# Performance work log

Measured on AMD Instinct MI355X. Metric: run time of the kernel, lower is better.

Reference implementation:

```python
import jax, jax.numpy as jnp
from jax import lax
import numpy as np


def conv2d(x, w, pad):
    # x: NCHW, w: OIHW
    return lax.conv_general_dilated(x, w, (1, 1), [(pad, pad), (pad, pad)],
                                    dimension_numbers=("NCHW", "OIHW", "NCHW"))


def make_dct_dict(num_atoms, num_dims):
    i = np.arange(num_atoms)[:, None].astype(np.float64)
    n = np.arange(num_dims)[None, :].astype(np.float64)
    w = np.cos((2.0 * n + 1.0) * i * (np.pi / (2.0 * num_dims)))
    w = w / np.linalg.norm(w, axis=1, keepdims=True)
    return jnp.asarray(w.T, dtype=jnp.float32)  # [num_dims, num_atoms]


def setup_inputs() -> dict:
    key = jax.random.key(0)
    B, C, H, W = 8, 64, 64, 64      # C = num_dims
    A = 256                          # num_atoms
    ks = jax.random.split(key, 10)
    s = 0.05
    Dict = make_dct_dict(A, C)       # [C, A]
    L = jnp.sum(Dict ** 2)           # ||Dict||_F^2 (scalar parameter)
    return {
        "x": jax.random.normal(ks[0], (B, C, H, W), jnp.float32),
        "conv_w": jax.random.normal(ks[1], (A, C, 3, 3), jnp.float32) * s,
        "conv_b": jax.random.normal(ks[2], (A,), jnp.float32) * s,
        "res1_w1": jax.random.normal(ks[3], (A // 2, A, 3, 3), jnp.float32) * s,
        "res1_w2": jax.random.normal(ks[4], (A, A // 2, 1, 1), jnp.float32) * s,
        "res2_w1": jax.random.normal(ks[5], (A // 2, A, 3, 3), jnp.float32) * s,
        "res2_w2": jax.random.normal(ks[6], (A, A // 2, 1, 1), jnp.float32) * s,
        "ca_w1": jax.random.normal(ks[7], (A // 16, A), jnp.float32) * s,  # Linear(A, A//16)
        "ca_w2": jax.random.normal(ks[8], (A, A // 16), jnp.float32) * s,  # Linear(A//16, A)
        "sa_w": jax.random.normal(ks[9], (1, 2, 3, 3), jnp.float32) * s,
        "Dict": Dict,
        "L": L,
        "num_iters": 16,
    }


def reference(x, conv_w, conv_b, res1_w1, res1_w2, res2_w1, res2_w2,
              ca_w1, ca_w2, sa_w, Dict, L, num_iters):
    def res_block(h, w1, w2):
        t = conv2d(jax.nn.relu(h), w1, 1)
        t = conv2d(jax.nn.relu(t), w2, 0)
        return h + t

    l = conv2d(x, conv_w, 1) + conv_b[None, :, None, None]
    l = res_block(l, res1_w1, res1_w2)
    l = res_block(l, res2_w1, res2_w2)

    # CBAM: channel attention (shared MLP on avg/max pooled features)
    avg = jnp.mean(l, axis=(2, 3))  # [B, A]
    mx = jnp.max(l, axis=(2, 3))
    fc = lambda v: jax.nn.relu(v @ ca_w1.T) @ ca_w2.T
    l = l * jax.nn.sigmoid(fc(avg) + fc(mx))[:, :, None, None]
    # CBAM: spatial attention
    s2 = jnp.concatenate([jnp.mean(l, axis=1, keepdims=True),
                          jnp.max(l, axis=1, keepdims=True)], axis=1)  # [B,2,H,W]
    l = l * jax.nn.sigmoid(conv2d(s2, sa_w, 1))

    lam = jnp.transpose(l / L, (0, 2, 3, 1))   # [B,H,W,A] per-position thresholds
    xp = jnp.transpose(x, (0, 2, 3, 1))        # [B,H,W,C]

    A = Dict.shape[1]
    S = (jnp.eye(A, dtype=Dict.dtype) - (Dict.T @ Dict) / L).T  # [A,A]
    y = xp @ Dict                               # [B,H,W,A]
    yL = y / L

    soft = lambda v: jnp.sign(v) * jnp.maximum(jnp.abs(v) - lam, 0.0)

    z0 = soft(y)

    def step(z, _):
        return soft(z @ S + yL), None

    z, _ = lax.scan(step, z0, None, length=num_iters)
    x_recon = z @ Dict.T                        # [B,H,W,C]

    return (jnp.transpose(z, (0, 3, 1, 2)),
            jnp.transpose(x_recon, (0, 3, 1, 2)),
            Dict)
```

## Files before the change

### kernel.cpp

```cpp
#include <hip/hip_runtime.h>
#include <hip/hip_bf16.h>

typedef __attribute__((ext_vector_type(8))) short short8v;
typedef __attribute__((ext_vector_type(4))) short short4v;
typedef __attribute__((ext_vector_type(4))) float float4v;

__device__ __forceinline__ unsigned short f2bu(float v){
  __hip_bfloat16 h = __float2bfloat16(v);
  union { __hip_bfloat16 h; unsigned short u; } cv; cv.h = h; return cv.u;
}

__device__ __forceinline__ float softt(float v, float lam){
  float t = fmaxf(fabsf(v) - lam, 0.f);
  float r = copysignf(t, v);
  return (v == 0.f) ? 0.f : r;
}

__global__ void k_Lin(const float* __restrict__ Lsrc, float* __restrict__ Lb){
  Lb[0] = Lsrc[0];
}

__global__ void k_gram(const float* __restrict__ D, unsigned short* __restrict__ Gb){
  int j = blockIdx.x, a = threadIdx.x;
  float acc = 0.f;
  for (int c = 0; c < 64; ++c)
    acc += D[c*256 + j] * D[c*256 + a];
  Gb[j*256 + a] = f2bu(acc);
}

__global__ void k_transpD(const float* __restrict__ D, float* __restrict__ DT,
                          unsigned short* __restrict__ DTb){
  int gid = blockIdx.x * 256 + threadIdx.x;
  if (gid < 16384) {
    int a = gid >> 6, c = gid & 63;
    float v = D[c*256 + a];
    DT[gid] = v;
    DTb[gid] = f2bu(v);
  }
}

__global__ void k_castw(const float* __restrict__ w, unsigned short* __restrict__ wb,
                        int n){
  int gid = blockIdx.x * 256 + threadIdx.x;
  if (gid < n) wb[gid] = f2bu(w[gid]);
}

__global__ void k_permw3(const float* __restrict__ w, unsigned short* __restrict__ wb,
                         int logI, int n){
  int gid = blockIdx.x * 256 + threadIdx.x;
  if (gid >= n) return;
  int I = 1 << logI;
  int i = gid & (I - 1);
  int t = gid >> logI;
  int o = t / 9;
  int r = t - o * 9;
  wb[gid] = f2bu(w[((o << logI) + i) * 9 + r]);
}

template<int KS, int CIN, int BN, bool BIAS, bool RES, bool WF32, bool WBF>
__global__ __launch_bounds__(256) void k_conv(
    const unsigned short* __restrict__ in, const unsigned short* __restrict__ wb,
    const float* __restrict__ bias, const float* res, float* outf,
    unsigned short* __restrict__ outb, int Cout)
{
  constexpr int TPC   = CIN / 64;
  constexpr int K     = KS * KS * CIN;
  constexpr int LOGBN = (BN == 128) ? 7 : 6;
  constexpr int BCH   = BN / 32;
  constexpr int NT    = BN / 64;

  __shared__ unsigned short Asb[64][72];
  __shared__ unsigned short Bsb[BN][72];

  const int tid = threadIdx.x;
  int bx = blockIdx.x;
  { const int cpx = gridDim.x >> 3; bx = (bx & 7) * cpx + (bx >> 3); }
  const int m0  = bx * 64;
  const int n0  = blockIdx.y * BN;
  const int b   = m0 >> 12;
  const int hw0 = m0 & 4095;
  const int h   = hw0 >> 6;
  const int w0  = hw0 & 63;

  const int sm  = tid & 63;
  const int sq8 = tid >> 6;
  const int bn  = tid & (BN - 1);
  const int bq  = tid >> LOGBN;

  const int w   = tid >> 6;
  const int ln  = tid & 63;
  const int q   = ln >> 4;
  const int l16 = ln & 15;

  float4v acc[NT][4];
  #pragma unroll
  for (int nt = 0; nt < NT; ++nt)
    #pragma unroll
    for (int mt = 0; mt < 4; ++mt)
      acc[nt][mt] = (float4v){0.f, 0.f, 0.f, 0.f};

  int sA = 0, sB = TPC;
  if (KS == 3) { sA = (h == 0 ? 3 : 0) * TPC; sB = (h == 63 ? 6 : 9) * TPC; }

  short8v a_r0, a_r1;
  short8v b_r[4];

  auto pref = [&](int s){
    const int r   = s / TPC;
    const int c64 = s - r * TPC;
    int hh = h, ww = w0 + sm;
    bool ok = true;
    if (KS == 3) {
      const int r3 = r / 3;
      const int dw = r - r3 * 3 - 1;
      hh = h + r3 - 1;
      ww += dw;
      ok = ((unsigned)ww < 64u);
    }
    a_r0 = (short8v){0,0,0,0,0,0,0,0};
    a_r1 = (short8v){0,0,0,0,0,0,0,0};
    if (ok) {
      const unsigned short* ap = in +
          (((size_t)(b * CIN + c64 * 64 + sq8 * 8)) << 12) + (hh << 6) + ww;
      #pragma unroll
      for (int j = 0; j < 8; ++j)
        a_r0[j] = (short)ap[(size_t)j << 12];
      const unsigned short* ap2 = ap + ((size_t)32 << 12);
      #pragma unroll
      for (int j = 0; j < 8; ++j)
        a_r1[j] = (short)ap2[(size_t)j << 12];
    }
    const unsigned short* bp = wb + (size_t)(n0 + bn) * K + s * 64 + bq * (BCH * 8);
    #pragma unroll
    for (int j = 0; j < BCH; ++j)
      b_r[j] = *(const short8v*)(bp + j * 8);
  };

  pref(sA);
  for (int s = sA; s < sB; ) {
    *(short8v*)(&Asb[sm][sq8 * 8])       = a_r0;
    *(short8v*)(&Asb[sm][32 + sq8 * 8])  = a_r1;
    #pragma unroll
    for (int j = 0; j < BCH; ++j)
      *(short8v*)(&Bsb[bn][bq * (BCH * 8) + j * 8]) = b_r[j];
    __syncthreads();
    const int sn = s + 1;
    if (sn < sB) pref(sn);
    short8v Af[4][2];
    #pragma unroll
    for (int mt = 0; mt < 4; ++mt) {
      Af[mt][0] = *(const short8v*)(&Asb[mt * 16 + l16][q * 8]);
      Af[mt][1] = *(const short8v*)(&Asb[mt * 16 + l16][32 + q * 8]);
    }
    #pragma unroll
    for (int nt = 0; nt < NT; ++nt) {
      const int nr = w * (BN / 4) + nt * 16 + l16;
      const short8v Bf0 = *(const short8v*)(&Bsb[nr][q * 8]);
      const short8v Bf1 = *(const short8v*)(&Bsb[nr][32 + q * 8]);
      #pragma unroll
      for (int mt = 0; mt < 4; ++mt) {
        acc[nt][mt] = __builtin_amdgcn_mfma_f32_16x16x32_bf16(
            Af[mt][0], Bf0, acc[nt][mt], 0, 0, 0);
        acc[nt][mt] = __builtin_amdgcn_mfma_f32_16x16x32_bf16(
            Af[mt][1], Bf1, acc[nt][mt], 0, 0, 0);
      }
    }
    __syncthreads();
    s = sn;
  }

  #pragma unroll
  for (int nt = 0; nt < NT; ++nt) {
    const int n = n0 + w * (BN / 4) + nt * 16 + l16;
    float bv = 0.f;
    if (BIAS) bv = bias[n];
    #pragma unroll
    for (int mt = 0; mt < 4; ++mt) {
      const size_t base = (((size_t)(b * Cout + n)) << 12) + hw0 + mt * 16 + q * 4;
      float o[4];
      #pragma unroll
      for (int r2 = 0; r2 < 4; ++r2) o[r2] = acc[nt][mt][r2] + bv;
      if (RES) {
        float4 r4 = *(const float4*)(res + base);
        o[0] += r4.x; o[1] += r4.y; o[2] += r4.z; o[3] += r4.w;
      }
      if (WF32) {
        float4 o4; o4.x = o[0]; o4.y = o[1]; o4.z = o[2]; o4.w = o[3];
        *(float4*)(outf + base) = o4;
      }
      if (WBF) {
        short4v s4;
        #pragma unroll
        for (int r2 = 0; r2 < 4; ++r2) s4[r2] = (short)f2bu(fmaxf(o[r2], 0.f));
        *(short4v*)(outb + base) = s4;
      }
    }
  }
}

__global__ void k_pool(const float* __restrict__ l, float* __restrict__ avg,
                       float* __restrict__ mx){
  int b = blockIdx.y, a = blockIdx.x, tid = threadIdx.x;
  const float* p = l + ((size_t)(b * 256 + a) << 12);
  float s = 0.f, m = -1e30f;
  for (int i = tid; i < 4096; i += 256) { float v = p[i]; s += v; m = fmaxf(m, v); }
  __shared__ float ss[256], sm[256];
  ss[tid] = s; sm[tid] = m; __syncthreads();
  for (int o = 128; o > 0; o >>= 1) {
    if (tid < o) { ss[tid] += ss[tid+o]; sm[tid] = fmaxf(sm[tid], sm[tid+o]); }
    __syncthreads();
  }
  if (tid == 0) { avg[b*256+a] = ss[0] * (1.f/4096.f); mx[b*256+a] = sm[0]; }
}

__global__ void k_ca(const float* __restrict__ avg, const float* __restrict__ mx,
                     const float* __restrict__ w1, const float* __restrict__ w2,
                     float* __restrict__ cscale){
  int b = blockIdx.x, tid = threadIdx.x;
  __shared__ float h[16];
  if (tid < 16) {
    float sa = 0.f, sm = 0.f;
    for (int a = 0; a < 256; ++a) {
      float w = w1[tid*256 + a];
      sa += avg[b*256 + a] * w;
      sm += mx[b*256 + a] * w;
    }
    h[tid] = fmaxf(sa, 0.f) + fmaxf(sm, 0.f);
  }
  __syncthreads();
  float s = 0.f;
  for (int j = 0; j < 16; ++j) s += h[j] * w2[tid*16 + j];
  cscale[b*256 + tid] = 1.f / (1.f + __expf(-s));
}

__global__ void k_s2(const float* __restrict__ l, const float* __restrict__ cscale,
                     float* __restrict__ s2){
  int b = blockIdx.y;
  int hw = blockIdx.x * 256 + threadIdx.x;
  const float* p  = l + (((size_t)b * 256) << 12) + hw;
  const float* cs = cscale + b * 256;
  float s = 0.f, m = -1e30f;
  for (int a = 0; a < 256; ++a) {
    float v = p[(size_t)a << 12] * cs[a];
    s += v; m = fmaxf(m, v);
  }
  s2[((b*2) << 12) + hw]   = s * (1.f/256.f);
  s2[((b*2+1) << 12) + hw] = m;
}

__global__ void k_sa(const float* __restrict__ s2, const float* __restrict__ w,
                     float* __restrict__ sa){
  int b = blockIdx.y;
  int hw = blockIdx.x * 256 + threadIdx.x;
  int h = hw >> 6, ww = hw & 63;
  float acc = 0.f;
  for (int ch = 0; ch < 2; ++ch)
    for (int dh = -1; dh <= 1; ++dh)
      for (int dw = -1; dw <= 1; ++dw) {
        int hh = h + dh, wc = ww + dw;
        if ((unsigned)hh < 64u && (unsigned)wc < 64u)
          acc += s2[((b*2+ch) << 12) + (hh << 6) + wc] * w[ch*9 + (dh+1)*3 + (dw+1)];
      }
  sa[(b << 12) + hw] = 1.f / (1.f + __expf(-acc));
}

#define XTS 80

__device__ __forceinline__ int zoff(int pos, int au8){
  return pos * 256 + (((au8 ^ (pos & 15)) & 31) << 3);
}

__global__ __launch_bounds__(256, 2) void k_lista(
    const unsigned short* __restrict__ xb,
    const unsigned short* __restrict__ DTb,
    const unsigned short* __restrict__ Gb,
    const float* __restrict__ lmap, const float* __restrict__ csc,
    const float* __restrict__ sav, const float* __restrict__ Lb,
    float* __restrict__ zout)
{
  __shared__ unsigned short zbuf[2][16 * 256];

  const int tid = threadIdx.x;
  const int m0  = blockIdx.x * 16;
  const int b   = m0 >> 12;
  const int hw0 = m0 & 4095;
  const float invL = 1.0f / Lb[0];

  unsigned short* xTb = &zbuf[1][0];
  {
    const int i  = tid & 15;
    const int c0 = tid >> 4;
    #pragma unroll
    for (int cc = 0; cc < 4; ++cc) {
      int c = c0 + cc * 16;
      xTb[i * XTS + c] = xb[((b * 64 + c) << 12) + hw0 + i];
    }
  }

  const int w   = tid >> 6;
  const int ln  = tid & 63;
  const int q   = ln >> 4;
  const int l16 = ln & 15;

  short8v Sg[4][8];
  #pragma unroll
  for (int at = 0; at < 4; ++at)
    #pragma unroll
    for (int ks = 0; ks < 8; ++ks)
      Sg[at][ks] = *(const short8v*)(
          Gb + (size_t)(w * 64 + at * 16 + l16) * 256 + ks * 32 + q * 8);

  __syncthreads();

  float z[4][4], yl[4][4], lamr[4][4];

  {
    const short8v B0 = *(const short8v*)(&xTb[l16 * XTS + q * 8]);
    const short8v B1 = *(const short8v*)(&xTb[l16 * XTS + 32 + q * 8]);
    #pragma unroll
    for (int at = 0; at < 4; ++at) {
      const int abase = w * 64 + at * 16;
      const short8v A0 = *(const short8v*)(DTb + (abase + l16) * 64 + q * 8);
      const short8v A1 = *(const short8v*)(DTb + (abase + l16) * 64 + 32 + q * 8);
      float4v a = {0.f, 0.f, 0.f, 0.f};
      a = __builtin_amdgcn_mfma_f32_16x16x32_bf16(A0, B0, a, 0, 0, 0);
      a = __builtin_amdgcn_mfma_f32_16x16x32_bf16(A1, B1, a, 0, 0, 0);
      short4v pk;
      #pragma unroll
      for (int r = 0; r < 4; ++r) {
        const int atom = abase + q * 4 + r;
        const float lv = lmap[(((size_t)(b * 256 + atom)) << 12) + hw0 + l16];
        const float sv = sav[(b << 12) + hw0 + l16];
        const float cv = csc[b * 256 + atom];
        const float lm = ((lv * cv) * sv) * invL;
        const float yv = a[r];
        lamr[at][r] = lm;
        yl[at][r]   = yv * invL;
        const float z0 = softt(yv, lm);
        z[at][r] = z0;
        pk[r] = (short)f2bu(z0);
      }
      *(short4v*)(&zbuf[0][zoff(l16, w * 8 + at * 2 + (q >> 1)) + (q & 1) * 4]) = pk;
    }
  }
  __syncthreads();

  int cur = 0;
  for (int it = 0; it < 16; ++it) {
    #pragma unroll
    for (int at = 0; at < 4; ++at)
      #pragma unroll
      for (int ks = 0; ks < 8; ++ks)
        asm volatile("" : "+v"(Sg[at][ks]));

    float4v acc[4];
    #pragma unroll
    for (int at = 0; at < 4; ++at)
      acc[at] = (float4v){0.f, 0.f, 0.f, 0.f};

    #pragma unroll
    for (int ks = 0; ks < 8; ++ks) {
      const short8v B = *(const short8v*)(&zbuf[cur][zoff(l16, ks * 4 + q)]);
      acc[0] = __builtin_amdgcn_mfma_f32_16x16x32_bf16(Sg[0][ks], B, acc[0], 0, 0, 0);
      acc[1] = __builtin_amdgcn_mfma_f32_16x16x32_bf16(Sg[1][ks], B, acc[1], 0, 0, 0);
      acc[2] = __builtin_amdgcn_mfma_f32_16x16x32_bf16(Sg[2][ks], B, acc[2], 0, 0, 0);
      acc[3] = __builtin_amdgcn_mfma_f32_16x16x32_bf16(Sg[3][ks], B, acc[3], 0, 0, 0);
    }

    #pragma unroll
    for (int at = 0; at < 4; ++at) {
      short4v pk;
      #pragma unroll
      for (int r = 0; r < 4; ++r) {
        const float u  = fmaf(-invL, acc[at][r], z[at][r] + yl[at][r]);
        const float nz = softt(u, lamr[at][r]);
        z[at][r] = nz;
        pk[r] = (short)f2bu(nz);
      }
      *(short4v*)(&zbuf[cur ^ 1][zoff(l16, w * 8 + at * 2 + (q >> 1)) + (q & 1) * 4]) = pk;
    }
    __syncthreads();
    cur ^= 1;
  }

  #pragma unroll
  for (int at = 0; at < 4; ++at) {
    float4 o;
    o.x = z[at][0]; o.y = z[at][1]; o.z = z[at][2]; o.w = z[at][3];
    *(float4*)(&zout[(size_t)(m0 + l16) * 256 + w * 64 + at * 16 + q * 4]) = o;
  }
}

__global__ __launch_bounds__(256) void k_recon_out(
    const float* __restrict__ z, const float* __restrict__ DT,
    float* __restrict__ out1, float* __restrict__ out0)
{
  __shared__ float zs[16][257];
  const int tid = threadIdx.x;
  const int r0  = blockIdx.x * 16;
  const int b   = r0 >> 12;
  const int hw0 = r0 & 4095;

  for (int idx = tid; idx < 4096; idx += 256) {
    int r = idx >> 8, k = idx & 255;
    zs[r][k] = z[(r0 + r) * 256 + k];
  }
  __syncthreads();

  for (int idx = tid; idx < 1024; idx += 256) {
    const int a  = idx >> 2;
    const int rr = (idx & 3) * 4;
    float4 o;
    o.x = zs[rr][a]; o.y = zs[rr+1][a]; o.z = zs[rr+2][a]; o.w = zs[rr+3][a];
    *(float4*)(&out0[(((size_t)(b * 256 + a)) << 12) + hw0 + rr]) = o;
  }

  const int c  = tid & 63;
  const int rg = tid >> 6;
  float acc[4] = {0.f, 0.f, 0.f, 0.f};
  for (int a = 0; a < 256; ++a) {
    float d = DT[a * 64 + c];
    #pragma unroll
    for (int i = 0; i < 4; ++i) acc[i] += zs[rg + 4*i][a] * d;
  }
  #pragma unroll
  for (int i = 0; i < 4; ++i) {
    int r = rg + 4*i;
    out1[((b * 64 + c) << 12) + hw0 + r] = acc[i];
  }
}

__global__ void k_dictout_f32(const float* __restrict__ D, float* __restrict__ out2){
  int i = blockIdx.x * 256 + threadIdx.x;
  if (i < 16384) out2[i] = D[i];
}

extern "C" void kernel_launch(void* const* d_in, const int* in_sizes, int n_in,
                              void* d_out, int out_size, void* d_ws, size_t ws_size,
                              hipStream_t stream)
{
  (void)in_sizes; (void)n_in; (void)out_size; (void)ws_size;

  const float* x    = (const float*)d_in[0];
  const float* cw   = (const float*)d_in[1];
  const float* cb   = (const float*)d_in[2];
  const float* r1w1 = (const float*)d_in[3];
  const float* r1w2 = (const float*)d_in[4];
  const float* r2w1 = (const float*)d_in[5];
  const float* r2w2 = (const float*)d_in[6];
  const float* caw1 = (const float*)d_in[7];
  const float* caw2 = (const float*)d_in[8];
  const float* saw  = (const float*)d_in[9];
  const float* D    = (const float*)d_in[10];
  const float* Lsrc = (const float*)d_in[11];

  float* p = (float*)d_ws;
  float* DT   = p; p += 16384;
  float* Lb   = p; p += 8;
  unsigned short* Gb  = (unsigned short*)p; p += 32768;
  unsigned short* DTb = (unsigned short*)p; p += 8192;
  unsigned short* cwb   = (unsigned short*)p; p += 73728;
  unsigned short* r1w1b = (unsigned short*)p; p += 147456;
  unsigned short* r1w2b = (unsigned short*)p; p += 16384;
  unsigned short* r2w1b = (unsigned short*)p; p += 147456;
  unsigned short* r2w2b = (unsigned short*)p; p += 16384;
  float* avg  = p; p += 2048;
  float* mx   = p; p += 2048;
  float* csc  = p; p += 2048;
  float* s2   = p; p += 65536;
  float* sa   = p; p += 32768;
  float* l    = p; p += 8388608;
  float* scr  = p; p += 8388608;
  float* zt   = p; p += 8388608;
  float* z    = zt;

  unsigned short* xb = (unsigned short*)scr;
  unsigned short* lb = (unsigned short*)(scr + 1048576);
  unsigned short* tb = (unsigned short*)(scr + 1048576 + 4194304);

  float* out0 = (float*)d_out;
  float* out1 = out0 + (size_t)8*256*4096;
  float* out2 = out1 + (size_t)8*64*4096;

  dim3 b256(256);

  k_Lin<<<dim3(1), dim3(1), 0, stream>>>(Lsrc, Lb);
  k_gram<<<dim3(256), b256, 0, stream>>>(D, Gb);
  k_transpD<<<dim3(64), b256, 0, stream>>>(D, DT, DTb);
  k_permw3<<<dim3(576),  b256, 0, stream>>>(cw,   cwb,   6, 147456);
  k_permw3<<<dim3(1152), b256, 0, stream>>>(r1w1, r1w1b, 8, 294912);
  k_castw <<<dim3(128),  b256, 0, stream>>>(r1w2, r1w2b, 32768);
  k_permw3<<<dim3(1152), b256, 0, stream>>>(r2w1, r2w1b, 8, 294912);
  k_castw <<<dim3(128),  b256, 0, stream>>>(r2w2, r2w2b, 32768);
  k_castw <<<dim3(8192), b256, 0, stream>>>(x, xb, 2097152);

  k_conv<3,  64, 128, true,  false, true,  true ><<<dim3(512, 2), b256, 0, stream>>>(
      xb, cwb, cb, (const float*)nullptr, l, lb, 256);
  k_conv<3, 256,  64, false, false, false, true ><<<dim3(512, 2), b256, 0, stream>>>(
      lb, r1w1b, (const float*)nullptr, (const float*)nullptr, (float*)nullptr, tb, 128);
  k_conv<1, 128, 128, false, true,  true,  true ><<<dim3(512, 2), b256, 0, stream>>>(
      tb, r1w2b, (const float*)nullptr, l, l, lb, 256);
  k_conv<3, 256,  64, false, false, false, true ><<<dim3(512, 2), b256, 0, stream>>>(
      lb, r2w1b, (const float*)nullptr, (const float*)nullptr, (float*)nullptr, tb, 128);
  k_conv<1, 128, 128, false, true,  true,  false><<<dim3(512, 2), b256, 0, stream>>>(
      tb, r2w2b, (const float*)nullptr, l, l, (unsigned short*)nullptr, 256);

  k_pool<<<dim3(256, 8), b256, 0, stream>>>(l, avg, mx);
  k_ca<<<dim3(8), b256, 0, stream>>>(avg, mx, caw1, caw2, csc);
  k_s2<<<dim3(16, 8), b256, 0, stream>>>(l, csc, s2);
  k_sa<<<dim3(16, 8), b256, 0, stream>>>(s2, saw, sa);

  k_lista<<<dim3(2048), b256, 0, stream>>>(xb, DTb, Gb, l, csc, sa, Lb, z);

  k_recon_out<<<dim3(2048), b256, 0, stream>>>(z, DT, out1, out0);
  k_dictout_f32<<<dim3(64), b256, 0, stream>>>(D, out2);
}
```

Before: 473.7 us.

## Store bf16 conv activations channels-last for vectorized im2col loads

Switches the bf16 input copy and the bf16 intermediate activations from NCHW to NHWC layout, using a new shared-memory transpose kernel for x. Conv A-operand prefetch then uses two 16-byte vector loads instead of sixteen strided 2-byte gathers, and the LISTA kernel loads x with vector loads. The cost is that the bf16 epilogue now writes scattered 2-byte stores strided by Cout, which may hurt write coalescing.

```diff
diff --git a/kernel.cpp b/kernel.cpp
--- a/kernel.cpp
+++ b/kernel.cpp
@@ -43,6 +43,30 @@
                         int n){
   int gid = blockIdx.x * 256 + threadIdx.x;
   if (gid < n) wb[gid] = f2bu(w[gid]);
+}
+
+__global__ __launch_bounds__(256) void k_castx_t(const float* __restrict__ x,
+                                                 unsigned short* __restrict__ xb){
+  __shared__ float zs[64][65];
+  const int tid = threadIdx.x;
+  const int hwt = blockIdx.x * 64;
+  const int b   = blockIdx.y;
+  const int j   = tid & 63;
+  const int c4  = tid >> 6;
+  #pragma unroll
+  for (int k = 0; k < 16; ++k) {
+    int c = c4 + k * 4;
+    zs[c][j] = x[((b * 64 + c) << 12) + hwt + j];
+  }
+  __syncthreads();
+  #pragma unroll
+  for (int hk = 0; hk < 2; ++hk) {
+    short8v v;
+    #pragma unroll
+    for (int e = 0; e < 8; ++e)
+      v[e] = (short)f2bu(zs[c4 * 16 + hk * 8 + e][j]);
+    *(short8v*)(&xb[((size_t)(b * 4096 + hwt + j)) * 64 + c4 * 16 + hk * 8]) = v;
+  }
 }
 
 __global__ void k_permw3(const float* __restrict__ w, unsigned short* __restrict__ wb,
@@ -121,14 +145,9 @@
     a_r1 = (short8v){0,0,0,0,0,0,0,0};
     if (ok) {
       const unsigned short* ap = in +
-          (((size_t)(b * CIN + c64 * 64 + sq8 * 8)) << 12) + (hh << 6) + ww;
-      #pragma unroll
-      for (int j = 0; j < 8; ++j)
-        a_r0[j] = (short)ap[(size_t)j << 12];
-      const unsigned short* ap2 = ap + ((size_t)32 << 12);
-      #pragma unroll
-      for (int j = 0; j < 8; ++j)
-        a_r1[j] = (short)ap2[(size_t)j << 12];
+          ((size_t)(b * 4096 + (hh << 6) + ww)) * CIN + c64 * 64 + sq8 * 8;
+      a_r0 = *(const short8v*)(ap);
+      a_r1 = *(const short8v*)(ap + 32);
     }
     const unsigned short* bp = wb + (size_t)(n0 + bn) * K + s * 64 + bq * (BCH * 8);
     #pragma unroll
@@ -176,23 +195,25 @@
     if (BIAS) bv = bias[n];
     #pragma unroll
     for (int mt = 0; mt < 4; ++mt) {
-      const size_t base = (((size_t)(b * Cout + n)) << 12) + hw0 + mt * 16 + q * 4;
+      const int pbase = hw0 + mt * 16 + q * 4;
       float o[4];
       #pragma unroll
       for (int r2 = 0; r2 < 4; ++r2) o[r2] = acc[nt][mt][r2] + bv;
       if (RES) {
+        const size_t base = (((size_t)(b * Cout + n)) << 12) + pbase;
         float4 r4 = *(const float4*)(res + base);
         o[0] += r4.x; o[1] += r4.y; o[2] += r4.z; o[3] += r4.w;
       }
       if (WF32) {
+        const size_t base = (((size_t)(b * Cout + n)) << 12) + pbase;
         float4 o4; o4.x = o[0]; o4.y = o[1]; o4.z = o[2]; o4.w = o[3];
         *(float4*)(outf + base) = o4;
       }
       if (WBF) {
-        short4v s4;
         #pragma unroll
-        for (int r2 = 0; r2 < 4; ++r2) s4[r2] = (short)f2bu(fmaxf(o[r2], 0.f));
-        *(short4v*)(outb + base) = s4;
+        for (int r2 = 0; r2 < 4; ++r2)
+          outb[((size_t)(b * 4096 + pbase + r2)) * Cout + n] =
+              f2bu(fmaxf(o[r2], 0.f));
       }
     }
   }
@@ -289,12 +310,9 @@
   unsigned short* xTb = &zbuf[1][0];
   {
     const int i  = tid & 15;
-    const int c0 = tid >> 4;
-    #pragma unroll
-    for (int cc = 0; cc < 4; ++cc) {
-      int c = c0 + cc * 16;
-      xTb[i * XTS + c] = xb[((b * 64 + c) << 12) + hw0 + i];
-    }
+    const int cg = tid >> 4;
+    *(short4v*)(&xTb[i * XTS + cg * 4]) =
+        *(const short4v*)(&xb[((size_t)(b * 4096 + hw0 + i)) * 64 + cg * 4]);
   }
 
   const int w   = tid >> 6;
@@ -492,7 +510,7 @@
   k_castw <<<dim3(128),  b256, 0, stream>>>(r1w2, r1w2b, 32768);
   k_permw3<<<dim3(1152), b256, 0, stream>>>(r2w1, r2w1b, 8, 294912);
   k_castw <<<dim3(128),  b256, 0, stream>>>(r2w2, r2w2b, 32768);
-  k_castw <<<dim3(8192), b256, 0, stream>>>(x, xb, 2097152);
+  k_castx_t<<<dim3(64, 8), b256, 0, stream>>>(x, xb);
 
   k_conv<3,  64, 128, true,  false, true,  true ><<<dim3(512, 2), b256, 0, stream>>>(
       xb, cwb, cb, (const float*)nullptr, l, lb, 256);
```

Result: slower. 505.7 us (+6.8%).
